# Kernel tuning notes

Hardware: AMD Instinct MI355X
Metric: run time of the kernel (lower is better)

Reference implementation:

```python
import jax, jax.numpy as jnp
import numpy as np

E = 8            # num_experts
PS = 8           # patch size (fixed across layers since ps-2 < 8)
F = 6            # fourier frequencies
CC = 4 + 8 * F   # coord feature channels = 52
RH = 16          # router hidden channels (embed_dim)
TEMP = 1.0
THRESH = 0.05
LAYERS = [(3, 8), (8, 16), (16, 16), (16, 32)]  # (C_in, C_out) per layer
NUM_CLASSES = 100


def coord_features(H, W, ps, nf):
    # [4+8F, H, W]: global (x,y) + patch-local (x,y) + sin/cos fourier bands
    gy = (jnp.arange(H, dtype=jnp.float32) + 0.5) / H
    gx = (jnp.arange(W, dtype=jnp.float32) + 0.5) / W
    ly = ((jnp.arange(H) % ps).astype(jnp.float32) + 0.5) / ps
    lx = ((jnp.arange(W) % ps).astype(jnp.float32) + 0.5) / ps
    Gy = jnp.broadcast_to(gy[:, None], (H, W))
    Gx = jnp.broadcast_to(gx[None, :], (H, W))
    Ly = jnp.broadcast_to(ly[:, None], (H, W))
    Lx = jnp.broadcast_to(lx[None, :], (H, W))
    base = jnp.stack([Gx, Gy, Lx, Ly], 0)  # [4,H,W]
    bands = [base]
    for f in range(nf):
        w = (2.0 ** f) * jnp.pi
        bands.append(jnp.sin(w * base))
        bands.append(jnp.cos(w * base))
    return jnp.concatenate(bands, 0)


def patchify(x, ps):
    B, C, H, W = x.shape
    h, w = H // ps, W // ps
    x = x.reshape(B, C, h, ps, w, ps).transpose(0, 2, 4, 1, 3, 5)
    return x.reshape(B, h * w, C, ps, ps), h, w


def unpatchify(x, h, w):
    # 'b (h w) c ph pw -> b c (h ph) (w pw)'
    B, P, C, ph, pw = x.shape
    return x.reshape(B, h, w, C, ph, pw).transpose(0, 3, 1, 4, 2, 5).reshape(B, C, h * ph, w * pw)


def pce_layer(X, ew, eb, rw, rb, rlw, rlb):
    B, C, H, W = X.shape
    Xp, h, w = patchify(X, PS)             # [B,P,C,ps,ps]
    P = h * w
    Xf = Xp.reshape(B * P, C, PS, PS)
    coords = coord_features(H, W, PS, F)   # [CC,H,W] (same for every image)
    Cp, _, _ = patchify(coords[None], PS)
    Cp = Cp[0]                             # [P,CC,ps,ps]
    # Router: 1x1 conv proj -> ReLU -> global avg pool -> linear -> softmax/temp -> threshold + renorm
    z = jax.nn.relu(jnp.einsum('rc,pcij->prij', rw, Cp) + rb[None, :, None, None])
    z = z.mean((2, 3))                     # [P,RH]
    logits = z @ rlw.T + rlb               # [P,E]
    probs = jax.nn.softmax(logits / TEMP, axis=-1)
    keep = (probs >= THRESH).astype(probs.dtype)
    probs = probs * keep
    probs = probs / (probs.sum(-1, keepdims=True) + 1e-9)
    scores = jnp.broadcast_to(probs[None], (B, P, E))  # [B,P,E]
    # Dense all-experts conv: stack experts along output channels of one conv
    y = jax.lax.conv_general_dilated(Xf, ew, (1, 1), 'SAME',
                                     dimension_numbers=('NCHW', 'OIHW', 'NCHW'))
    y = jax.nn.relu(y + eb[None, :, None, None])       # [B*P, E*Cout, ps, ps]
    Cout = ew.shape[0] // E
    y = y.reshape(B, P, E, Cout, PS, PS)
    out = jnp.einsum('bpecij,bpe->bpcij', y, scores)   # weighted combine over experts
    return unpatchify(out, h, w)


def setup_inputs() -> dict:
    key = jax.random.key(0)
    ks = jax.random.split(key, 32)
    d = {'X': jax.random.normal(ks[0], (16, 3, 128, 128), dtype=jnp.float32)}
    ki = 1
    for li, (cin, cout) in enumerate(LAYERS):
        d[f'ew{li}'] = jax.random.normal(ks[ki], (E * cout, cin, 3, 3), dtype=jnp.float32) * (1.0 / np.sqrt(cin * 9)); ki += 1
        d[f'eb{li}'] = jax.random.normal(ks[ki], (E * cout,), dtype=jnp.float32) * 0.01; ki += 1
        d[f'rw{li}'] = jax.random.normal(ks[ki], (RH, CC), dtype=jnp.float32) * (1.0 / np.sqrt(CC)); ki += 1
        d[f'rb{li}'] = jax.random.normal(ks[ki], (RH,), dtype=jnp.float32) * 0.01; ki += 1
        d[f'rlw{li}'] = jax.random.normal(ks[ki], (E, RH), dtype=jnp.float32) * (1.0 / np.sqrt(RH)); ki += 1
        d[f'rlb{li}'] = jax.random.normal(ks[ki], (E,), dtype=jnp.float32) * 0.01; ki += 1
    d['fcw'] = jax.random.normal(ks[ki], (NUM_CLASSES, LAYERS[-1][1] * 8 * 8), dtype=jnp.float32) * 0.02; ki += 1
    d['fcb'] = jnp.zeros((NUM_CLASSES,), dtype=jnp.float32)
    return d


def reference(X, ew0, eb0, rw0, rb0, rlw0, rlb0,
              ew1, eb1, rw1, rb1, rlw1, rlb1,
              ew2, eb2, rw2, rb2, rlw2, rlb2,
              ew3, eb3, rw3, rb3, rlw3, rlb3,
              fcw, fcb):
    layer_params = [(ew0, eb0, rw0, rb0, rlw0, rlb0),
                    (ew1, eb1, rw1, rb1, rlw1, rlb1),
                    (ew2, eb2, rw2, rb2, rlw2, rlb2),
                    (ew3, eb3, rw3, rb3, rlw3, rlb3)]
    for p in layer_params:
        X = pce_layer(X, *p)
    B, C, H, W = X.shape
    # AdaptiveAvgPool2d(8): exact 16x16 mean pooling for 128x128
    pooled = X.reshape(B, C, 8, H // 8, 8, W // 8).mean((3, 5))
    flat = pooled.reshape(B, -1)
    return flat @ fcw.T + fcb
```

## Files before the change

### kernel.cpp

```cpp
#include <hip/hip_runtime.h>
#include <math.h>

#define NE 8
#define PI_F 3.14159265358979323846f

typedef _Float16 half8 __attribute__((ext_vector_type(8)));
typedef float f32x4 __attribute__((ext_vector_type(4)));
typedef float f32x16 __attribute__((ext_vector_type(16)));
typedef unsigned int uint2v __attribute__((ext_vector_type(2)));
typedef unsigned int u32x4 __attribute__((ext_vector_type(4)));
typedef unsigned short u16x4 __attribute__((ext_vector_type(4)));

#define CP 24
#define ROWS 240
#define NELEM 2400

__device__ __forceinline__ unsigned short f2h_bits(float v) {
    union { _Float16 h; unsigned short u; } cv;
    cv.h = (_Float16)v;
    return cv.u;
}

struct SetupArgs {
    const float* rw[4]; const float* rb[4]; const float* rlw[4]; const float* rlb[4];
    const float* ew[4];
    float* probs;
    unsigned short* w0; unsigned short* w1; unsigned short* w2; unsigned short* w3;
};

template<int CIN, int CSTR, int KSL>
__device__ __forceinline__ void prep_one32(
    const float* __restrict__ ew, unsigned short* __restrict__ wA, int idx)
{
    int j    = idx & 7;
    int lane = (idx >> 3) & 63;
    int t2   = idx >> 9;
    int ks   = t2 % KSL;
    int mt   = t2 / KSL;
    int m    = mt * 32 + (lane & 31);
    int k    = ks * 16 + (lane >> 5) * 8 + j;
    int cin  = k % CSTR, r = k / CSTR;
    float val = 0.0f;
    if (cin < CIN && r < 9)
        val = ew[((size_t)m * CIN + cin) * 9 + r];
    wA[idx] = f2h_bits(val);
}

__global__ __launch_bounds__(256) void setup_all(SetupArgs sa)
{
    int bx = blockIdx.x, tid = threadIdx.x;
    if (bx < 256) {
        int layer = tid >> 6, lane = tid & 63;
        const float* rw  = sa.rw[layer];  const float* rb  = sa.rb[layer];
        const float* rlw = sa.rlw[layer]; const float* rlb = sa.rlb[layer];
        int p = bx, py = p >> 4, px = p & 15;
        int i = lane >> 3, j = lane & 7;
        int y = py * 8 + i, x = px * 8 + j;

        float base0 = (x + 0.5f) / 128.0f;
        float base1 = (y + 0.5f) / 128.0f;
        float base2 = (j + 0.5f) / 8.0f;
        float base3 = (i + 0.5f) / 8.0f;

        float coord[52];
        coord[0] = base0; coord[1] = base1; coord[2] = base2; coord[3] = base3;
        int c = 4;
        #pragma unroll
        for (int f = 0; f < 6; ++f) {
            float w = PI_F * (float)(1 << f);
            coord[c+0] = sinf(w * base0); coord[c+1] = sinf(w * base1);
            coord[c+2] = sinf(w * base2); coord[c+3] = sinf(w * base3);
            coord[c+4] = cosf(w * base0); coord[c+5] = cosf(w * base1);
            coord[c+6] = cosf(w * base2); coord[c+7] = cosf(w * base3);
            c += 8;
        }
        float z[16];
        #pragma unroll
        for (int r = 0; r < 16; ++r) {
            float a = rb[r];
            #pragma unroll
            for (int cc = 0; cc < 52; ++cc) a += rw[r*52 + cc] * coord[cc];
            z[r] = fmaxf(a, 0.0f);
        }
        #pragma unroll
        for (int r = 0; r < 16; ++r) {
            float v = z[r];
            #pragma unroll
            for (int off = 32; off > 0; off >>= 1) v += __shfl_xor(v, off);
            z[r] = v * (1.0f / 64.0f);
        }
        int e = lane & 7;
        float logit = rlb[e];
        #pragma unroll
        for (int r = 0; r < 16; ++r) logit += rlw[e*16 + r] * z[r];
        float m = logit;
        #pragma unroll
        for (int off = 4; off > 0; off >>= 1) m = fmaxf(m, __shfl_xor(m, off));
        float ex = expf(logit - m);
        float s = ex;
        #pragma unroll
        for (int off = 4; off > 0; off >>= 1) s += __shfl_xor(s, off);
        float pr = ex / s;
        pr = (pr >= 0.05f) ? pr : 0.0f;
        float s2 = pr;
        #pragma unroll
        for (int off = 4; off > 0; off >>= 1) s2 += __shfl_xor(s2, off);
        pr = pr / (s2 + 1e-9f);
        if (lane < 8) sa.probs[layer * 2048 + p * 8 + lane] = pr;
    } else {
        int idx = (bx - 256) * 256 + tid;
        if (idx < 3072)       prep_one32<3, 4, 3>(sa.ew[0], sa.w0, idx);
        else if (idx < 13312) prep_one32<8, 8, 5>(sa.ew[1], sa.w1, idx - 3072);
        else if (idx < 31744) prep_one32<16, 16, 9>(sa.ew[2], sa.w2, idx - 13312);
        else if (idx < 68608) prep_one32<16, 16, 9>(sa.ew[3], sa.w3, idx - 31744);
    }
}

template<int KSL, int CSTR>
__device__ __forceinline__ void build_B32(
    half8* B, const unsigned short* ain, int n, int hi)
{
    int pr = n >> 3, pc = n & 7;
    int rbase = pr * ROWS + pc * CP;
    if (CSTR == 16) {
        #pragma unroll
        for (int ks = 0; ks < KSL; ++ks) {
            int off = ((ks / 3) * 10 + (ks % 3)) * CP + hi * 8;
            B[ks] = *(const half8*)(ain + rbase + off);
        }
    } else if (CSTR == 8) {
        #pragma unroll
        for (int ks = 0; ks < KSL; ++ks) {
            int r0 = 2 * ks, r1 = 2 * ks + 1;
            int o0 = ((r0 / 3) * 10 + (r0 % 3)) * CP;
            int o1 = (r1 < 9) ? ((r1 / 3) * 10 + (r1 % 3)) * CP : 0;
            int off = hi ? o1 : o0;
            half8 v{};
            if (2 * ks + hi < 9) v = *(const half8*)(ain + rbase + off);
            B[ks] = v;
        }
    } else {
        #pragma unroll
        for (int ks = 0; ks < KSL; ++ks) {
            union { half8 v; uint2v u2[2]; } bb;
            #pragma unroll
            for (int h = 0; h < 2; ++h) {
                int ra = 4 * ks + h;
                int rb_ = 4 * ks + 2 + h;
                int oa = (ra < 9) ? ((ra / 3) * 10 + (ra % 3)) * CP : 0;
                int ob = (rb_ < 9) ? ((rb_ / 3) * 10 + (rb_ % 3)) * CP : 0;
                int r = 4 * ks + 2 * hi + h;
                int off = hi ? ob : oa;
                uint2v u{};
                if (r < 9) u = *(const uint2v*)(ain + rbase + off);
                bb.u2[h] = u;
            }
            B[ks] = bb.v;
        }
    }
}

template<int KSL, int CSTR, int MT, int CPE, bool LAST>
__device__ __forceinline__ void layer_nt(
    const unsigned short* Ain, unsigned short* Aout,
    const unsigned short* __restrict__ wA,
    const float* sbR_L, const float* se_L,
    int l, int hi, int l31, int nt, f32x16& accL)
{
    int n = nt * 32 + l31;
    half8 B[KSL];
    build_B32<KSL, CSTR>(B, Ain, n, hi);

    constexpr int KH0 = (KSL + 1) / 2;
    constexpr int KH1 = KSL - KH0;

    f32x4 acc_a = {0,0,0,0}, acc_b = {0,0,0,0};
    f32x4 acc_s = {0,0,0,0};

    const unsigned short* apl = wA + l * 8;
    half8 A0[KH0], A1[KH1 > 0 ? KH1 : 1];
    #pragma unroll
    for (int q = 0; q < KH0; ++q)
        A0[q] = *(const half8*)(apl + q * 512);

    #pragma unroll 1
    for (int mt = 0; mt < MT; ++mt) {
        const unsigned short* base = apl + mt * (KSL * 512);
        #pragma unroll
        for (int q = 0; q < KH1; ++q)
            A1[q] = *(const half8*)(base + (KH0 + q) * 512);

        const float* bp = sbR_L + mt * 32 + hi * 16;
        f32x4 b0 = *(const f32x4*)(bp);
        f32x4 b1 = *(const f32x4*)(bp + 4);
        f32x4 b2 = *(const f32x4*)(bp + 8);
        f32x4 b3 = *(const f32x4*)(bp + 12);
        f32x16 ct;
        #pragma unroll
        for (int i = 0; i < 4; ++i) {
            ct[i] = b0[i]; ct[4+i] = b1[i]; ct[8+i] = b2[i]; ct[12+i] = b3[i];
        }

        #pragma unroll
        for (int q = 0; q < KH0; ++q)
            ct = __builtin_amdgcn_mfma_f32_32x32x16_f16(A0[q], B[q], ct, 0, 0, 0);

        const unsigned short* nbase = apl + ((mt + 1 < MT) ? (mt + 1) : 0) * (KSL * 512);
        #pragma unroll
        for (int q = 0; q < KH0; ++q)
            A0[q] = *(const half8*)(nbase + q * 512);

        #pragma unroll
        for (int q = 0; q < KH1; ++q)
            ct = __builtin_amdgcn_mfma_f32_32x32x16_f16(A1[q], B[KH0 + q], ct, 0, 0, 0);

        if (CPE == 32) {
            float pe = se_L[mt];
            #pragma unroll
            for (int g = 0; g < 16; ++g)
                accL[g] = fmaf(fmaxf(ct[g], 0.f), pe, accL[g]);
        } else if (CPE == 16) {
            float pe0 = se_L[2 * mt], pe1 = se_L[2 * mt + 1];
            #pragma unroll
            for (int g = 0; g < 4; ++g) {
                acc_a[g] = fmaf(fmaxf(ct[g],      0.f), pe0, acc_a[g]);
                acc_a[g] = fmaf(fmaxf(ct[8 + g],  0.f), pe1, acc_a[g]);
                acc_b[g] = fmaf(fmaxf(ct[4 + g],  0.f), pe0, acc_b[g]);
                acc_b[g] = fmaf(fmaxf(ct[12 + g], 0.f), pe1, acc_b[g]);
            }
        } else {
            #pragma unroll
            for (int q = 0; q < 4; ++q) {
                float pe = se_L[4 * mt + q];
                #pragma unroll
                for (int g = 0; g < 4; ++g)
                    acc_s[g] = fmaf(fmaxf(ct[4 * q + g], 0.f), pe, acc_s[g]);
            }
        }
    }

    if (!LAST) {
        int wb = (1 + (n >> 3)) * ROWS + (1 + (n & 7)) * CP;
        union { _Float16 h[4]; u16x4 u; } o;
        if (CPE == 8) {
            #pragma unroll
            for (int g = 0; g < 4; ++g) o.h[g] = (_Float16)acc_s[g];
            *(u16x4*)(Aout + wb + 4 * hi) = o.u;
        } else {
            #pragma unroll
            for (int g = 0; g < 4; ++g) o.h[g] = (_Float16)acc_a[g];
            *(u16x4*)(Aout + wb + 4 * hi) = o.u;
            #pragma unroll
            for (int g = 0; g < 4; ++g) o.h[g] = (_Float16)acc_b[g];
            *(u16x4*)(Aout + wb + 8 + 4 * hi) = o.u;
        }
    }
}

__global__ __launch_bounds__(128, 3) void pce_fused(
    const float* __restrict__ X,
    const unsigned short* __restrict__ wA0, const unsigned short* __restrict__ wA1,
    const unsigned short* __restrict__ wA2, const unsigned short* __restrict__ wA3,
    const float* __restrict__ eb0, const float* __restrict__ eb1,
    const float* __restrict__ eb2, const float* __restrict__ eb3,
    const float* __restrict__ probs,
    float* __restrict__ psums)
{
    int bx = blockIdx.x;
    int b = bx >> 7;
    int pbase = (bx & 127) << 1;
    int tid = threadIdx.x;
    int w = tid >> 6, l = tid & 63;
    int p = pbase + w;
    int py = p >> 4, px = p & 15;

    __shared__ alignas(16) unsigned short A[2][2][NELEM];
    __shared__ alignas(16) float sbR[576];
    __shared__ alignas(16) float se[4][2][8];

    if (tid < 64) {
        int layer = tid >> 4, q = (tid >> 3) & 1, e = tid & 7;
        se[layer][q][e] = probs[layer * 2048 + (pbase + q) * 8 + e];
    }
    for (int t = tid; t < 576; t += 128) {
        const float* ebp; int off;
        if (t < 64)       { ebp = eb0; off = 0; }
        else if (t < 192) { ebp = eb1; off = 64; }
        else if (t < 320) { ebp = eb2; off = 192; }
        else              { ebp = eb3; off = 320; }
        int local = t - off;
        int mt = local >> 5, q = local & 31;
        int hi2 = q >> 4, reg = q & 15;
        int row = (reg & 3) + 8 * (reg >> 2) + 4 * hi2;
        sbR[t] = ebp[mt * 32 + row];
    }

    unsigned short* Aping = A[w][0];
    unsigned short* Apong = A[w][1];
    {
        u32x4 z = {0u, 0u, 0u, 0u};
        for (int t = l; t < 300; t += 64) {
            ((u32x4*)Aping)[t] = z;
            ((u32x4*)Apong)[t] = z;
        }
        for (int t = l; t < 192; t += 64) {
            int cin = t >> 6, pix = t & 63, i = pix >> 3, j = pix & 7;
            float v = X[((size_t)(b * 3 + cin) * 128 + (py * 8 + i)) * 128 + (px * 8 + j)];
            Aping[(1 + i) * ROWS + (1 + j) * CP + cin] = f2h_bits(v);
        }
    }
    __syncthreads();

    int l31 = l & 31, hi = l >> 5;
    f32x16 accL = {0.f};

    layer_nt<3, 4, 2, 8, false>(Aping, Apong, wA0, sbR,       se[0][w], l, hi, l31, 0, accL);
    layer_nt<3, 4, 2, 8, false>(Aping, Apong, wA0, sbR,       se[0][w], l, hi, l31, 1, accL);
    layer_nt<5, 8, 4, 16, false>(Apong, Aping, wA1, sbR + 64,  se[1][w], l, hi, l31, 0, accL);
    layer_nt<5, 8, 4, 16, false>(Apong, Aping, wA1, sbR + 64,  se[1][w], l, hi, l31, 1, accL);
    layer_nt<9, 16, 4, 16, false>(Aping, Apong, wA2, sbR + 192, se[2][w], l, hi, l31, 0, accL);
    layer_nt<9, 16, 4, 16, false>(Aping, Apong, wA2, sbR + 192, se[2][w], l, hi, l31, 1, accL);
    layer_nt<9, 16, 8, 32, true>(Apong, Aping, wA3, sbR + 320, se[3][w], l, hi, l31, 0, accL);
    layer_nt<9, 16, 8, 32, true>(Apong, Aping, wA3, sbR + 320, se[3][w], l, hi, l31, 1, accL);

    float* pout = psums + (size_t)(b * 256 + p) * 32;
    #pragma unroll
    for (int g = 0; g < 16; ++g) {
        float s = accL[g];
        s += __shfl_xor(s, 1);  s += __shfl_xor(s, 2);
        s += __shfl_xor(s, 4);  s += __shfl_xor(s, 8);
        s += __shfl_xor(s, 16);
        accL[g] = s;
    }
    if (l31 == 0) {
        #pragma unroll
        for (int qd = 0; qd < 4; ++qd) {
            f32x4 v = { accL[4*qd], accL[4*qd+1], accL[4*qd+2], accL[4*qd+3] };
            *(f32x4*)(pout + qd * 8 + 4 * hi) = v;
        }
    }
}

__global__ __launch_bounds__(256) void fc_kernel(
    const float* __restrict__ psums, const float* __restrict__ fcw,
    const float* __restrict__ fcb, float* __restrict__ out)
{
    int b = blockIdx.x >> 3, chunk = blockIdx.x & 7;
    __shared__ float pooled[2048];
    for (int t = threadIdx.x; t < 2048; t += 256) {
        int c = t >> 6, cell = t & 63, oy = cell >> 3, ox = cell & 7;
        float s = 0.0f;
        #pragma unroll
        for (int dy = 0; dy < 2; ++dy)
            #pragma unroll
            for (int dx = 0; dx < 2; ++dx) {
                int pp = (2 * oy + dy) * 16 + (2 * ox + dx);
                s += psums[(size_t)(b * 256 + pp) * 32 + c];
            }
        pooled[t] = s * (1.0f / 256.0f);
    }
    __syncthreads();

    int wave = threadIdx.x >> 6, lane = threadIdx.x & 63;
    for (int ci = wave; ci < 13; ci += 4) {
        int cls = chunk * 13 + ci;
        if (cls < 100) {
            float a = 0.0f;
            #pragma unroll
            for (int r = 0; r < 32; ++r)
                a += pooled[r * 64 + lane] * fcw[(size_t)cls * 2048 + r * 64 + lane];
            #pragma unroll
            for (int off = 32; off > 0; off >>= 1) a += __shfl_down(a, off);
            if (lane == 0) out[b * 100 + cls] = a + fcb[cls];
        }
    }
}

extern "C" void kernel_launch(void* const* d_in, const int* in_sizes, int n_in,
                              void* d_out, int out_size, void* d_ws, size_t ws_size,
                              hipStream_t stream) {
    const float* X = (const float*)d_in[0];
    const float* eb[4];
    SetupArgs sa;
    for (int l = 0; l < 4; ++l) {
        sa.ew[l]  = (const float*)d_in[1 + 6*l + 0];
        eb[l]     = (const float*)d_in[1 + 6*l + 1];
        sa.rw[l]  = (const float*)d_in[1 + 6*l + 2];
        sa.rb[l]  = (const float*)d_in[1 + 6*l + 3];
        sa.rlw[l] = (const float*)d_in[1 + 6*l + 4];
        sa.rlb[l] = (const float*)d_in[1 + 6*l + 5];
    }
    const float* fcw = (const float*)d_in[25];
    const float* fcb = (const float*)d_in[26];

    char* ws = (char*)d_ws;
    float* probs  = (float*)ws;
    float* psums  = (float*)(ws + 32768);
    unsigned short* wA0 = (unsigned short*)(ws + 32768 + 524288);
    unsigned short* wA1 = wA0 + 3072;
    unsigned short* wA2 = wA1 + 10240;
    unsigned short* wA3 = wA2 + 18432;

    sa.probs = probs; sa.w0 = wA0; sa.w1 = wA1; sa.w2 = wA2; sa.w3 = wA3;

    setup_all<<<524, 256, 0, stream>>>(sa);
    pce_fused<<<2048, 128, 0, stream>>>(X, wA0, wA1, wA2, wA3,
                                        eb[0], eb[1], eb[2], eb[3], probs, psums);
    fc_kernel<<<128, 256, 0, stream>>>(psums, fcw, fcb, (float*)d_out);
}
```

Before: 80.12 us.

## Chunk expert weight prefetch into ping-pong buffers and raise occupancy bound

Reworks the per-expert MFMA loop so the A-operand weights are loaded in chunks of three K-slices, alternating between two small register buffers. Each chunk is prefetched one step ahead, across pairs of expert tiles. It also raises the launch-bounds minimum blocks per CU from 3 to 4. The aim is to cut register pressure from holding half of K in registers, so more waves fit and weight load latency is hidden at a finer grain. The tighter register budget could force spills. The loop also assumes MT is even.

```diff
diff --git a/kernel.cpp b/kernel.cpp
--- a/kernel.cpp
+++ b/kernel.cpp
@@ -171,70 +171,87 @@
     half8 B[KSL];
     build_B32<KSL, CSTR>(B, Ain, n, hi);
 
-    constexpr int KH0 = (KSL + 1) / 2;
-    constexpr int KH1 = KSL - KH0;
+    constexpr int NC = (KSL + 2) / 3;
 
     f32x4 acc_a = {0,0,0,0}, acc_b = {0,0,0,0};
     f32x4 acc_s = {0,0,0,0};
 
     const unsigned short* apl = wA + l * 8;
-    half8 A0[KH0], A1[KH1 > 0 ? KH1 : 1];
+    half8 Aa[3], Ab[3];
+
     #pragma unroll
-    for (int q = 0; q < KH0; ++q)
-        A0[q] = *(const half8*)(apl + q * 512);
+    for (int q = 0; q < ((KSL < 3) ? KSL : 3); ++q)
+        Aa[q] = *(const half8*)(apl + q * 512);
 
     #pragma unroll 1
-    for (int mt = 0; mt < MT; ++mt) {
-        const unsigned short* base = apl + mt * (KSL * 512);
-        #pragma unroll
-        for (int q = 0; q < KH1; ++q)
-            A1[q] = *(const half8*)(base + (KH0 + q) * 512);
-
-        const float* bp = sbR_L + mt * 32 + hi * 16;
-        f32x4 b0 = *(const f32x4*)(bp);
-        f32x4 b1 = *(const f32x4*)(bp + 4);
-        f32x4 b2 = *(const f32x4*)(bp + 8);
-        f32x4 b3 = *(const f32x4*)(bp + 12);
-        f32x16 ct;
-        #pragma unroll
-        for (int i = 0; i < 4; ++i) {
-            ct[i] = b0[i]; ct[4+i] = b1[i]; ct[8+i] = b2[i]; ct[12+i] = b3[i];
-        }
-
-        #pragma unroll
-        for (int q = 0; q < KH0; ++q)
-            ct = __builtin_amdgcn_mfma_f32_32x32x16_f16(A0[q], B[q], ct, 0, 0, 0);
-
-        const unsigned short* nbase = apl + ((mt + 1 < MT) ? (mt + 1) : 0) * (KSL * 512);
-        #pragma unroll
-        for (int q = 0; q < KH0; ++q)
-            A0[q] = *(const half8*)(nbase + q * 512);
-
-        #pragma unroll
-        for (int q = 0; q < KH1; ++q)
-            ct = __builtin_amdgcn_mfma_f32_32x32x16_f16(A1[q], B[KH0 + q], ct, 0, 0, 0);
-
-        if (CPE == 32) {
-            float pe = se_L[mt];
-            #pragma unroll
-            for (int g = 0; g < 16; ++g)
-                accL[g] = fmaf(fmaxf(ct[g], 0.f), pe, accL[g]);
-        } else if (CPE == 16) {
-            float pe0 = se_L[2 * mt], pe1 = se_L[2 * mt + 1];
-            #pragma unroll
-            for (int g = 0; g < 4; ++g) {
-                acc_a[g] = fmaf(fmaxf(ct[g],      0.f), pe0, acc_a[g]);
-                acc_a[g] = fmaf(fmaxf(ct[8 + g],  0.f), pe1, acc_a[g]);
-                acc_b[g] = fmaf(fmaxf(ct[4 + g],  0.f), pe0, acc_b[g]);
-                acc_b[g] = fmaf(fmaxf(ct[12 + g], 0.f), pe1, acc_b[g]);
+    for (int mtp = 0; mtp < MT; mtp += 2) {
+        #pragma unroll
+        for (int halfI = 0; halfI < 2; ++halfI) {
+            int mt = mtp + halfI;
+            const float* bp = sbR_L + mt * 32 + hi * 16;
+            f32x4 b0 = *(const f32x4*)(bp);
+            f32x4 b1 = *(const f32x4*)(bp + 4);
+            f32x4 b2 = *(const f32x4*)(bp + 8);
+            f32x4 b3 = *(const f32x4*)(bp + 12);
+            f32x16 ct;
+            #pragma unroll
+            for (int i = 0; i < 4; ++i) {
+                ct[i] = b0[i]; ct[4+i] = b1[i]; ct[8+i] = b2[i]; ct[12+i] = b3[i];
             }
-        } else {
-            #pragma unroll
-            for (int q = 0; q < 4; ++q) {
-                float pe = se_L[4 * mt + q];
+
+            #pragma unroll
+            for (int c = 0; c < NC; ++c) {
+                const int t  = halfI * NC + c;
+                const int tn = t + 1;
+                {
+                    const int ncidx = (tn >= 2 * NC) ? 0 : (tn % NC);
+                    const int CHN = (ncidx == NC - 1) ? (KSL - 3 * (NC - 1)) : 3;
+                    int tmt;
+                    if (tn >= 2 * NC)   tmt = (mtp + 2 < MT) ? (mtp + 2) : 0;
+                    else if (tn >= NC)  tmt = mtp + 1;
+                    else                tmt = mtp;
+                    const unsigned short* pfb =
+                        apl + ((size_t)tmt * KSL + 3 * ncidx) * 512;
+                    if ((tn & 1) == 0) {
+                        #pragma unroll
+                        for (int q = 0; q < CHN; ++q)
+                            Aa[q] = *(const half8*)(pfb + q * 512);
+                    } else {
+                        #pragma unroll
+                        for (int q = 0; q < CHN; ++q)
+                            Ab[q] = *(const half8*)(pfb + q * 512);
+                    }
+                }
+                const int CHC = (c == NC - 1) ? (KSL - 3 * (NC - 1)) : 3;
                 #pragma unroll
-                for (int g = 0; g < 4; ++g)
-                    acc_s[g] = fmaf(fmaxf(ct[4 * q + g], 0.f), pe, acc_s[g]);
+                for (int q = 0; q < CHC; ++q) {
+                    half8 a = ((t & 1) == 0) ? Aa[q] : Ab[q];
+                    ct = __builtin_amdgcn_mfma_f32_32x32x16_f16(a, B[3 * c + q], ct, 0, 0, 0);
+                }
+            }
+
+            if (CPE == 32) {
+                float pe = se_L[mt];
+                #pragma unroll
+                for (int g = 0; g < 16; ++g)
+                    accL[g] = fmaf(fmaxf(ct[g], 0.f), pe, accL[g]);
+            } else if (CPE == 16) {
+                float pe0 = se_L[2 * mt], pe1 = se_L[2 * mt + 1];
+                #pragma unroll
+                for (int g = 0; g < 4; ++g) {
+                    acc_a[g] = fmaf(fmaxf(ct[g],      0.f), pe0, acc_a[g]);
+                    acc_a[g] = fmaf(fmaxf(ct[8 + g],  0.f), pe1, acc_a[g]);
+                    acc_b[g] = fmaf(fmaxf(ct[4 + g],  0.f), pe0, acc_b[g]);
+                    acc_b[g] = fmaf(fmaxf(ct[12 + g], 0.f), pe1, acc_b[g]);
+                }
+            } else {
+                #pragma unroll
+                for (int q = 0; q < 4; ++q) {
+                    float pe = se_L[4 * mt + q];
+                    #pragma unroll
+                    for (int g = 0; g < 4; ++g)
+                        acc_s[g] = fmaf(fmaxf(ct[4 * q + g], 0.f), pe, acc_s[g]);
+                }
             }
         }
     }
@@ -257,7 +274,7 @@
     }
 }
 
-__global__ __launch_bounds__(128, 3) void pce_fused(
+__global__ __launch_bounds__(128, 4) void pce_fused(
     const float* __restrict__ X,
     const unsigned short* __restrict__ wA0, const unsigned short* __restrict__ wA1,
     const unsigned short* __restrict__ wA2, const unsigned short* __restrict__ wA3,
```

Result: slower. 85.92 us (+7.2%).
